# Kernel optimization log

Measured on AMD Instinct MI355X. Metric: run time of the kernel, lower is better.

The kernel has to match this reference:

```python
import jax, jax.numpy as jnp
import numpy as np


def setup_inputs() -> dict:
    key = jax.random.key(0)
    k1, k2, k3, k4 = jax.random.split(key, 4)
    n, c, p1, p2, r = 8, 3, 512, 512, 8
    X = jax.random.uniform(k1, (n, c, p1, p2), dtype=jnp.float32)
    S = jax.random.uniform(k2, (c, r), dtype=jnp.float32)
    S = S / (jnp.linalg.norm(S, axis=0, keepdims=True))  # unit-norm columns like S_init
    gamma = jax.random.uniform(k3, (1,), dtype=jnp.float32) * 1e-05
    lam = jax.random.uniform(k4, (1,), dtype=jnp.float32) * 1e-05
    return {"X": X, "S": S, "gamma": gamma, "lam": lam, "n_iter": 2}


def reference(X, S, gamma, lam, n_iter):
    n, c, p1, p2 = X.shape
    p = p1 * p2
    r = S.shape[1]
    Xf = X.reshape(n, c, p)
    gamma = jnp.abs(gamma)
    lam = jnp.abs(lam)
    Dt = jnp.zeros((n, r, p), dtype=X.dtype)
    x0 = jnp.mean(Xf, axis=2, keepdims=True)
    for _ in range(n_iter):
        # ---- D update (proximal gradient) ----
        SDt = jnp.einsum('cr,nrp->ncp', S, Dt)  # S @ Dt
        x0 = jnp.mean(Xf + SDt, axis=2, keepdims=True)  # [n,c,1]
        tau_D = 1.0 / jnp.sum(S * S)  # 1/||S||_F^2
        Dt = Dt - tau_D * jnp.einsum('cr,ncp->nrp', S, SDt + Xf - x0)
        S_nrm = jnp.linalg.norm(S, axis=0).reshape(1, r, 1)  # [1,r,1]
        Dt = jax.nn.relu(Dt - lam * gamma * tau_D * S_nrm)
        Dt_L2 = jnp.linalg.norm(Dt, axis=2, keepdims=True)  # [n,r,1]
        scl = jax.nn.relu(Dt_L2 - lam * tau_D * S_nrm)
        scl = scl / Dt_L2 + 1e-10  # faithful to source (eps added after divide)
        Dt = Dt * scl
        # ---- S update (proximal gradient) ----
        SDt = jnp.einsum('cr,nrp->ncp', S, Dt)
        x0 = jnp.mean(Xf + SDt, axis=2, keepdims=True)
        Dt_sum = jnp.sum(Dt, axis=2, keepdims=True)  # [n,r,1]
        tau_S = 1.0 / jnp.mean(jnp.sum(Dt * Dt, axis=(1, 2)))
        grad = jnp.mean(
            jnp.einsum('ncp,nqp->ncq', SDt + Xf, Dt)
            - x0 @ jnp.transpose(Dt_sum, (0, 2, 1)),
            axis=0)  # [c,r]
        S_grad = S - tau_S * grad
        Dt_nrm = jnp.mean(
            gamma * jnp.sum(jnp.abs(Dt), axis=2, keepdims=True)
            + jnp.linalg.norm(Dt, axis=2, keepdims=True), axis=0)  # [r,1]
        Sg_nrm = jnp.linalg.norm(S_grad, axis=0, keepdims=True)  # [1,r]
        scl_S = jax.nn.relu(Sg_nrm - lam * tau_S * Dt_nrm.T)
        scl_S = scl_S / (Sg_nrm + 1e-10)
        S = S_grad * scl_S
        # ---- unit-norm rescale (unit_norm_S=True) ----
        S_nrm2 = jnp.linalg.norm(S, axis=0, keepdims=True)  # [1,r]
        S = S / (S_nrm2 + 1e-10)
        Dt = Dt * (S_nrm2.reshape(1, r, 1) + 1e-10)
    return x0, S, Dt.reshape(n, r, p1, p2)
```

## Files before the change

kernel.cpp:

```cpp
#include <hip/hip_runtime.h>

constexpr int N = 8, C = 3, R = 8;
constexpr int P = 512 * 512;
constexpr int BLK = 256;
constexpr int NB = 128;
constexpr int PPB = P / NB;
constexpr int PITER = PPB / (BLK * 4);
constexpr int NK = 68;

typedef float f32x4 __attribute__((ext_vector_type(4)));

constexpr int W_XMEAN = 0;
constexpr int W_S0    = 32;
constexpr int W_S1    = 64;
constexpr int W_S2    = 96;
constexpr int W_X01   = 128;
constexpr int W_X02   = 160;
constexpr int W_F1    = 192;
constexpr int W_F2    = 256;
constexpr int W_TAU1  = 320;
constexpr int W_TAU2  = 321;
constexpr int W_THR1  = 328;
constexpr int W_THR2  = 336;
constexpr int W_SNRM1 = 344;
constexpr int W_SNRM2 = 352;
constexpr int W_RED   = 384;
constexpr int W_PXF   = 1024;
constexpr int W_PART  = 2560;

#define XR8(M) M(0) M(1) M(2) M(3) M(4) M(5) M(6) M(7)
#define XTRI(M) \
  M(0,0) \
  M(1,0) M(1,1) \
  M(2,0) M(2,1) M(2,2) \
  M(3,0) M(3,1) M(3,2) M(3,3) \
  M(4,0) M(4,1) M(4,2) M(4,3) M(4,4) \
  M(5,0) M(5,1) M(5,2) M(5,3) M(5,4) M(5,5) \
  M(6,0) M(6,1) M(6,2) M(6,3) M(6,4) M(6,5) M(6,6) \
  M(7,0) M(7,1) M(7,2) M(7,3) M(7,4) M(7,5) M(7,6) M(7,7)
#define XCR(M) \
  M(0,0) M(0,1) M(0,2) M(0,3) M(0,4) M(0,5) M(0,6) M(0,7) \
  M(1,0) M(1,1) M(1,2) M(1,3) M(1,4) M(1,5) M(1,6) M(1,7) \
  M(2,0) M(2,1) M(2,2) M(2,3) M(2,4) M(2,5) M(2,6) M(2,7)

__device__ __forceinline__ float sld(float x) {
    return __uint_as_float(__builtin_amdgcn_readfirstlane(__float_as_uint(x)));
}

__device__ __forceinline__ float waveSum(float v) {
    #pragma unroll
    for (int o = 32; o > 0; o >>= 1) v += __shfl_down(v, o);
    return v;
}

__global__ __launch_bounds__(BLK)
void k_xmean(const float* __restrict__ X, float* __restrict__ ws) {
    int nc = blockIdx.y;
    int t = threadIdx.x;
    size_t base = (size_t)nc * P + (size_t)blockIdx.x * 4096;
    float s = 0.f;
    #pragma unroll
    for (int i = 0; i < 4; ++i) {
        float4 q = *(const float4*)(X + base + (size_t)(i * BLK + t) * 4);
        s += (q.x + q.y) + (q.z + q.w);
    }
    __shared__ float red[4];
    s = waveSum(s);
    int lane = t & 63, wid = t >> 6;
    if (lane == 0) red[wid] = s;
    __syncthreads();
    if (t == 0) ws[W_PXF + nc * 64 + blockIdx.x] = (red[0] + red[1]) + (red[2] + red[3]);
}

__global__ void k_init(float* __restrict__ ws, const float* __restrict__ Sin,
                       const float* __restrict__ gp, const float* __restrict__ lp) {
    int t = threadIdx.x;
    __shared__ float sS[C * R];
    __shared__ float tau1;
    if (t < N * C) {
        float s = 0.f;
        for (int j = 0; j < 64; ++j) s += ws[W_PXF + t * 64 + j];
        float xm = s * (1.0f / P);
        ws[W_XMEAN + t] = xm;
        ws[W_X01 + t] = xm;
    }
    if (t < C * R) { sS[t] = Sin[t]; ws[W_S0 + t] = Sin[t]; }
    __syncthreads();
    if (t == 0) {
        float ssq = 0.f;
        for (int i = 0; i < C * R; ++i) ssq += sS[i] * sS[i];
        tau1 = 1.0f / ssq;
        ws[W_TAU1] = tau1;
    }
    __syncthreads();
    if (t < R) {
        float s2 = 0.f;
        #pragma unroll
        for (int c = 0; c < C; ++c) { float v = sS[c * R + t]; s2 += v * v; }
        float nrm = sqrtf(s2);
        ws[W_SNRM1 + t] = nrm;
        ws[W_THR1 + t] = fabsf(*lp) * fabsf(*gp) * tau1 * nrm;
    }
}

template <int MODE>
__global__ __launch_bounds__(BLK, 1)
void k_dpass(const float* __restrict__ X, const float* __restrict__ ws,
             float* __restrict__ part, float* __restrict__ Dt_out) {
    const int n = blockIdx.y, t = threadIdx.x;

#define LD_S0(c,q) const float S0_##c##q = sld(ws[W_S0 + (c) * R + (q)]);
#define LD_S1(c,q) const float S1_##c##q = sld(ws[W_S1 + (c) * R + (q)]);
    XCR(LD_S0)
    XCR(LD_S1)
#define LD_TH1(r) const float th1_##r = sld(ws[W_THR1 + (r)]);
#define LD_TH2(r) const float th2_##r = sld(ws[W_THR2 + (r)]);
#define LD_F1(r)  const float f1_##r  = sld(ws[W_F1 + n * R + (r)]);
#define LD_F2(r)  const float f2_##r  = sld(ws[W_F2 + n * R + (r)]);
    XR8(LD_TH1) XR8(LD_TH2) XR8(LD_F1) XR8(LD_F2)
    const float tau1c = sld(ws[W_TAU1]), tau2c = sld(ws[W_TAU2]);
    const float x01_0 = sld(ws[W_X01 + n * C + 0]);
    const float x01_1 = sld(ws[W_X01 + n * C + 1]);
    const float x01_2 = sld(ws[W_X01 + n * C + 2]);
    const float dx0_0 = sld(x01_0 - ws[W_X02 + n * C + 0]);
    const float dx0_1 = sld(x01_1 - ws[W_X02 + n * C + 1]);
    const float dx0_2 = sld(x01_2 - ws[W_X02 + n * C + 2]);

#define D_SM(r)   float sm_##r = 0.f;
#define D_T(q,r)  float tq_##q##_##r = 0.f;
#define D_V(c,q)  float vv_##c##_##q = 0.f;
    XR8(D_SM) XTRI(D_T) XCR(D_V)

    const float* Xn = X + (size_t)n * C * P;
    float* Dn = Dt_out + (size_t)n * R * P;

#define C_P1(r) const float p_##r = fmaxf(fmaf(-tau1c, fmaf(S0_0##r, tt0, fmaf(S0_1##r, tt1, S0_2##r * tt2)), -th1_##r), 0.f);
#define C_AL(r) const float a_##r = p_##r;
#define C_D2(r) const float d_##r = f1_##r * p_##r;
#define C_W(c)  const float w##c = fmaf(S1_##c##0, d_0, fmaf(S1_##c##1, d_1, fmaf(S1_##c##2, d_2, fmaf(S1_##c##3, d_3, fmaf(S1_##c##4, d_4, fmaf(S1_##c##5, d_5, fmaf(S1_##c##6, d_6, fmaf(S1_##c##7, d_7, tt##c + dx0_##c))))))));
#define C_A2(r) const float a_##r = fmaxf(fmaf(-tau2c, fmaf(S1_0##r, w0, fmaf(S1_1##r, w1, S1_2##r * w2)), d_##r - th2_##r), 0.f);
#define AC_SM(r)  sm_##r += a_##r;
#define AC_T(q,r) tq_##q##_##r = fmaf(a_##r, a_##q, tq_##q##_##r);
#define AC_V(c,q) vv_##c##_##q = fmaf(tt##c, a_##q, vv_##c##_##q);
#define PXc(r) ov_##r.x = f2_##r * a_##r;
#define PYc(r) ov_##r.y = f2_##r * a_##r;
#define PZc(r) ov_##r.z = f2_##r * a_##r;
#define PWc(r) ov_##r.w = f2_##r * a_##r;
#define GXc(q) (q).x
#define GYc(q) (q).y
#define GZc(q) (q).z
#define GWc(q) (q).w

#define SITE(GET, PUTM) { \
    const float tt0 = GET(xv0) - x01_0; \
    const float tt1 = GET(xv1) - x01_1; \
    const float tt2 = GET(xv2) - x01_2; \
    XR8(C_P1) \
    if constexpr (MODE == 0) { \
        XR8(C_AL) XR8(AC_SM) XTRI(AC_T) XCR(AC_V) \
    } else { \
        XR8(C_D2) C_W(0) C_W(1) C_W(2) XR8(C_A2) \
        if constexpr (MODE == 1) { XR8(AC_SM) XTRI(AC_T) XCR(AC_V) } \
        else { XR8(PUTM) } \
    } }

#define D_OV(r) float4 ov_##r;
#define ST_O(r) { f32x4 wv = { ov_##r.x, ov_##r.y, ov_##r.z, ov_##r.w }; \
                  __builtin_nontemporal_store(wv, (f32x4*)(Dn + (size_t)(r) * P + pbase)); }

    #pragma unroll
    for (int it = 0; it < PITER; ++it) {
        size_t pbase = (size_t)blockIdx.x * PPB + (size_t)(it * BLK + t) * 4;
        float4 xv0 = *(const float4*)(Xn + 0 * (size_t)P + pbase);
        float4 xv1 = *(const float4*)(Xn + 1 * (size_t)P + pbase);
        float4 xv2 = *(const float4*)(Xn + 2 * (size_t)P + pbase);
        XR8(D_OV)
        SITE(GXc, PXc)
        SITE(GYc, PYc)
        SITE(GZc, PZc)
        SITE(GWc, PWc)
        if constexpr (MODE == 2) { XR8(ST_O) }
    }

    if constexpr (MODE < 2) {
        __shared__ float red[4 * NK];
        const int lane = t & 63, wid = t >> 6;
#define RD_SM(r)  { float v = waveSum(sm_##r);       if (lane == 0) red[wid * NK + (r)] = v; }
#define RD_T(q,r) { float v = waveSum(tq_##q##_##r); if (lane == 0) red[wid * NK + 8 + (q) * ((q) + 1) / 2 + (r)] = v; }
#define RD_V(c,q) { float v = waveSum(vv_##c##_##q); if (lane == 0) red[wid * NK + 44 + (c) * R + (q)] = v; }
        XR8(RD_SM) XTRI(RD_T) XCR(RD_V)
        __syncthreads();
        for (int k = t; k < NK; k += BLK)
            part[((size_t)k * N + n) * NB + blockIdx.x] =
                (red[k] + red[NK + k]) + (red[2 * NK + k] + red[3 * NK + k]);
    }
}

__global__ __launch_bounds__(64)
void k_red(const float* __restrict__ part, float* __restrict__ ws) {
    int g = blockIdx.x, t = threadIdx.x;
    const float* p = part + (size_t)g * NB;
    float s = p[t] + p[t + 64];
    s = waveSum(s);
    if (t == 0) ws[W_RED + g] = s;
}

template <int IT>
__global__ __launch_bounds__(64)
void k_t23(float* __restrict__ ws, const float* __restrict__ gp,
           const float* __restrict__ lp, float* __restrict__ x0_out,
           float* __restrict__ S_out) {
    int t = threadIdx.x;
    __shared__ float sum_[N][R], T_[N][R][R], U_[N][C][R];
    __shared__ float scl_[N][R], L2_[N][R], x0s_[N][C], dtn_[R], x01_[N * C];
    __shared__ float Scur_[C * R], Snew_[C * R], grad_[C * R], snrm2_[R];
    __shared__ float tauS_, lam_, gam_, tauD_;
    for (int i = t; i < NK * N; i += 64) {
        int k = i / N, n = i % N;
        float v = ws[W_RED + k * N + n];
        if (k < 8) sum_[n][k] = v;
        else if (k < 44) {
            int m = k - 8;
            int q = 0;
            while ((q + 1) * (q + 2) / 2 <= m) ++q;
            int r = m - q * (q + 1) / 2;
            T_[n][r][q] = v; T_[n][q][r] = v;
        } else {
            int m = k - 44;
            U_[n][m >> 3][m & 7] = v;
        }
    }
    if (t < N * C) x01_[t] = ws[W_X01 + t];
    if (t == 0) {
        lam_ = fabsf(*lp); gam_ = fabsf(*gp);
        tauD_ = ws[IT ? W_TAU2 : W_TAU1];
    }
    if (t < C * R) Scur_[t] = ws[(IT ? W_S1 : W_S0) + t];
    __syncthreads();
    for (int i = t; i < N * C * R; i += 64) {
        int n = i / (C * R), m = i % (C * R);
        int c = m >> 3, q = m & 7;
        U_[n][c][q] += x01_[n * C + c] * sum_[n][q];
    }
    if (t < N * R) {
        int n = t >> 3, r = t & 7;
        float l2 = sqrtf(T_[n][r][r]);
        float snrm = ws[(IT ? W_SNRM2 : W_SNRM1) + r];
        float scl = fmaxf(l2 - lam_ * tauD_ * snrm, 0.f) / l2 + 1e-10f;
        scl_[n][r] = scl; L2_[n][r] = l2;
    }
    __syncthreads();
    if (t == 0) {
        float tot = 0.f;
        for (int n = 0; n < N; ++n)
            for (int r = 0; r < R; ++r)
                tot += scl_[n][r] * scl_[n][r] * T_[n][r][r];
        tauS_ = (float)N / tot;
    }
    if (t < N * C) {
        int n = t / C, c = t % C;
        float acc = ws[W_XMEAN + t];
        #pragma unroll
        for (int r = 0; r < R; ++r)
            acc += Scur_[c * R + r] * scl_[n][r] * sum_[n][r] * (1.0f / P);
        x0s_[n][c] = acc;
        if (IT == 1) x0_out[t] = acc;
    }
    if (t >= 32 && t < 32 + R) {
        int r = t - 32;
        float a = 0.f;
        #pragma unroll
        for (int n = 0; n < N; ++n)
            a += scl_[n][r] * (gam_ * sum_[n][r] + L2_[n][r]);
        dtn_[r] = a * (1.0f / N);
    }
    __syncthreads();
    if (t < C * R) {
        int c = t / R, q = t % R;
        float a = 0.f;
        #pragma unroll
        for (int n = 0; n < N; ++n) {
            float m = U_[n][c][q];
            #pragma unroll
            for (int r = 0; r < R; ++r)
                m += Scur_[c * R + r] * scl_[n][r] * T_[n][r][q];
            a += scl_[n][q] * (m - x0s_[n][c] * sum_[n][q]);
        }
        grad_[t] = a * (1.0f / N);
    }
    __syncthreads();
    if (t == 0) {
        float Sg[C * R], Sn[C * R];
        #pragma unroll
        for (int i = 0; i < C * R; ++i) Sg[i] = Scur_[i] - tauS_ * grad_[i];
        #pragma unroll
        for (int q = 0; q < R; ++q) {
            float s2 = 0.f;
            #pragma unroll
            for (int c = 0; c < C; ++c) s2 += Sg[c * R + q] * Sg[c * R + q];
            float sgn = sqrtf(s2);
            float s = fmaxf(sgn - lam_ * tauS_ * dtn_[q], 0.f) / (sgn + 1e-10f);
            #pragma unroll
            for (int c = 0; c < C; ++c) Sn[c * R + q] = Sg[c * R + q] * s;
        }
        #pragma unroll
        for (int q = 0; q < R; ++q) {
            float s2 = 0.f;
            #pragma unroll
            for (int c = 0; c < C; ++c) s2 += Sn[c * R + q] * Sn[c * R + q];
            float n2 = sqrtf(s2);
            snrm2_[q] = n2;
            #pragma unroll
            for (int c = 0; c < C; ++c) {
                float v = Sn[c * R + q] / (n2 + 1e-10f);
                Snew_[c * R + q] = v;
                ws[(IT ? W_S2 : W_S1) + c * R + q] = v;
                if (IT == 1) S_out[c * R + q] = v;
            }
        }
        if (IT == 0) {
            float ssq = 0.f;
            #pragma unroll
            for (int i = 0; i < C * R; ++i) ssq += Snew_[i] * Snew_[i];
            float tau2 = 1.0f / ssq;
            ws[W_TAU2] = tau2;
            #pragma unroll
            for (int r = 0; r < R; ++r) {
                float s2 = 0.f;
                #pragma unroll
                for (int c = 0; c < C; ++c) s2 += Snew_[c * R + r] * Snew_[c * R + r];
                float nrm = sqrtf(s2);
                ws[W_SNRM2 + r] = nrm;
                ws[W_THR2 + r] = lam_ * gam_ * tau2 * nrm;
            }
        }
    }
    __syncthreads();
    if (t < N * R) {
        float ft = scl_[t >> 3][t & 7] * (snrm2_[t & 7] + 1e-10f);
        ws[(IT ? W_F2 : W_F1) + t] = ft;
    }
    __syncthreads();
    if (IT == 0 && t < N * C) {
        int n = t / C, c = t % C;
        float acc = ws[W_XMEAN + t];
        #pragma unroll
        for (int r = 0; r < R; ++r)
            acc += Snew_[c * R + r] * ws[W_F1 + n * R + r] * sum_[n][r] * (1.0f / P);
        ws[W_X02 + t] = acc;
    }
}

extern "C" void kernel_launch(void* const* d_in, const int* in_sizes, int n_in,
                              void* d_out, int out_size, void* d_ws, size_t ws_size,
                              hipStream_t stream) {
    const float* X   = (const float*)d_in[0];
    const float* Sin = (const float*)d_in[1];
    const float* gam = (const float*)d_in[2];
    const float* lam = (const float*)d_in[3];
    float* out    = (float*)d_out;
    float* x0_out = out;
    float* S_out  = out + 24;
    float* Dt_out = out + 48;
    float* ws     = (float*)d_ws;
    float* part   = ws + W_PART;

    k_xmean<<<dim3(64, N * C), BLK, 0, stream>>>(X, ws);
    k_init<<<1, 64, 0, stream>>>(ws, Sin, gam, lam);

    k_dpass<0><<<dim3(NB, N), BLK, 0, stream>>>(X, ws, part, Dt_out);
    k_red<<<NK * N, 64, 0, stream>>>(part, ws);
    k_t23<0><<<1, 64, 0, stream>>>(ws, gam, lam, x0_out, S_out);

    k_dpass<1><<<dim3(NB, N), BLK, 0, stream>>>(X, ws, part, Dt_out);
    k_red<<<NK * N, 64, 0, stream>>>(part, ws);
    k_t23<1><<<1, 64, 0, stream>>>(ws, gam, lam, x0_out, S_out);

    k_dpass<2><<<dim3(NB, N), BLK, 0, stream>>>(X, ws, part, Dt_out);
}
```

Measured before the change: 100.5 us.

## Fold reduction and small-matrix update kernels into each dpass prologue

Drops the k_init, k_red and k_t23 kernels. Every dpass block now reduces the previous pass's partial sums itself and redundantly recomputes the small S/scale update, so each iteration is one launch instead of three. The block count is halved (NB 128→64) to shrink the partial-sum arrays each block must read, and ping-pong buffers keep reads and writes apart. In exchange every block repeats about 544 row reductions plus the serial t23 math, and the grid has fewer blocks to spread the streaming work across.

```diff
diff --git a/kernel.cpp b/kernel.cpp
--- a/kernel.cpp
+++ b/kernel.cpp
@@ -3,7 +3,7 @@
 constexpr int N = 8, C = 3, R = 8;
 constexpr int P = 512 * 512;
 constexpr int BLK = 256;
-constexpr int NB = 128;
+constexpr int NB = 64;
 constexpr int PPB = P / NB;
 constexpr int PITER = PPB / (BLK * 4);
 constexpr int NK = 68;
@@ -11,22 +11,15 @@
 typedef float f32x4 __attribute__((ext_vector_type(4)));
 
 constexpr int W_XMEAN = 0;
-constexpr int W_S0    = 32;
-constexpr int W_S1    = 64;
-constexpr int W_S2    = 96;
-constexpr int W_X01   = 128;
+constexpr int W_S1    = 32;
+constexpr int W_F1    = 64;
+constexpr int W_THR2  = 128;
+constexpr int W_TAU2  = 136;
+constexpr int W_SNRM2 = 144;
 constexpr int W_X02   = 160;
-constexpr int W_F1    = 192;
-constexpr int W_F2    = 256;
-constexpr int W_TAU1  = 320;
-constexpr int W_TAU2  = 321;
-constexpr int W_THR1  = 328;
-constexpr int W_THR2  = 336;
-constexpr int W_SNRM1 = 344;
-constexpr int W_SNRM2 = 352;
-constexpr int W_RED   = 384;
-constexpr int W_PXF   = 1024;
-constexpr int W_PART  = 2560;
+constexpr int W_PXF   = 256;
+constexpr int W_PA    = 2048;
+constexpr int W_PB    = 36864;
 
 #define XR8(M) M(0) M(1) M(2) M(3) M(4) M(5) M(6) M(7)
 #define XTRI(M) \
@@ -46,7 +39,6 @@
 __device__ __forceinline__ float sld(float x) {
     return __uint_as_float(__builtin_amdgcn_readfirstlane(__float_as_uint(x)));
 }
-
 __device__ __forceinline__ float waveSum(float v) {
     #pragma unroll
     for (int o = 32; o > 0; o >>= 1) v += __shfl_down(v, o);
@@ -72,59 +64,217 @@
     if (t == 0) ws[W_PXF + nc * 64 + blockIdx.x] = (red[0] + red[1]) + (red[2] + red[3]);
 }
 
-__global__ void k_init(float* __restrict__ ws, const float* __restrict__ Sin,
-                       const float* __restrict__ gp, const float* __restrict__ lp) {
-    int t = threadIdx.x;
-    __shared__ float sS[C * R];
-    __shared__ float tau1;
-    if (t < N * C) {
-        float s = 0.f;
-        for (int j = 0; j < 64; ++j) s += ws[W_PXF + t * 64 + j];
-        float xm = s * (1.0f / P);
-        ws[W_XMEAN + t] = xm;
-        ws[W_X01 + t] = xm;
-    }
-    if (t < C * R) { sS[t] = Sin[t]; ws[W_S0 + t] = Sin[t]; }
-    __syncthreads();
+template <int IT>
+__device__ void t23_math(const float* __restrict__ redL, const float* __restrict__ Sin,
+                         const float* __restrict__ ws, float lam_, float gam_,
+                         float* oS, float* oF, float* oTH2, float* oTAU2,
+                         float* oX02, float* oSN2, float* ox0s) {
+    const int t = threadIdx.x;
+    __shared__ float sum_[N][R], T_[N][R][R], U_[N][C][R];
+    __shared__ float scl_[N][R], L2_[N][R], x0s_[N][C], dtn_[R];
+    __shared__ float Scur_[24], grad_[24], snrm_in[8];
+    __shared__ float tauS_, tauD_;
+    for (int i = t; i < NK * N; i += BLK) {
+        int k = i / N, nn = i % N;
+        float v = redL[k * N + nn];
+        if (k < 8) sum_[nn][k] = v;
+        else if (k < 44) {
+            int m = k - 8; int q = 0;
+            while ((q + 1) * (q + 2) / 2 <= m) ++q;
+            int r = m - q * (q + 1) / 2;
+            T_[nn][r][q] = v; T_[nn][q][r] = v;
+        } else { int m = k - 44; U_[nn][m >> 3][m & 7] = v; }
+    }
+    if (t < 24) Scur_[t] = IT ? ws[W_S1 + t] : Sin[t];
     if (t == 0) {
-        float ssq = 0.f;
-        for (int i = 0; i < C * R; ++i) ssq += sS[i] * sS[i];
-        tau1 = 1.0f / ssq;
-        ws[W_TAU1] = tau1;
-    }
-    __syncthreads();
-    if (t < R) {
-        float s2 = 0.f;
-        #pragma unroll
-        for (int c = 0; c < C; ++c) { float v = sS[c * R + t]; s2 += v * v; }
-        float nrm = sqrtf(s2);
-        ws[W_SNRM1 + t] = nrm;
-        ws[W_THR1 + t] = fabsf(*lp) * fabsf(*gp) * tau1 * nrm;
-    }
+        if (IT) tauD_ = ws[W_TAU2];
+        else { float s = 0.f; for (int i = 0; i < 24; ++i) s += Sin[i] * Sin[i]; tauD_ = 1.0f / s; }
+    }
+    if (t < 8) {
+        if (IT) snrm_in[t] = ws[W_SNRM2 + t];
+        else snrm_in[t] = sqrtf(Sin[t] * Sin[t] + Sin[8 + t] * Sin[8 + t] + Sin[16 + t] * Sin[16 + t]);
+    }
+    __syncthreads();
+    for (int i = t; i < N * C * R; i += BLK) {
+        int nn = i / 24, m = i % 24, c = m >> 3, q = m & 7;
+        U_[nn][c][q] += ws[W_XMEAN + nn * 3 + c] * sum_[nn][q];
+    }
+    if (t < 64) {
+        int nn = t >> 3, r = t & 7;
+        float l2 = sqrtf(T_[nn][r][r]);
+        float scl = fmaxf(l2 - lam_ * tauD_ * snrm_in[r], 0.f) / l2 + 1e-10f;
+        scl_[nn][r] = scl; L2_[nn][r] = l2;
+    }
+    __syncthreads();
+    if (t == 0) {
+        float tot = 0.f;
+        for (int nn = 0; nn < N; ++nn)
+            for (int r = 0; r < R; ++r)
+                tot += scl_[nn][r] * scl_[nn][r] * T_[nn][r][r];
+        tauS_ = (float)N / tot;
+    }
+    if (t < 24) {
+        int nn = t / 3, c = t % 3;
+        float acc = ws[W_XMEAN + t];
+        #pragma unroll
+        for (int r = 0; r < R; ++r)
+            acc += Scur_[c * R + r] * scl_[nn][r] * sum_[nn][r] * (1.0f / P);
+        x0s_[nn][c] = acc;
+        if (IT == 1) ox0s[t] = acc;
+    }
+    if (t >= 32 && t < 40) {
+        int r = t - 32;
+        float a = 0.f;
+        #pragma unroll
+        for (int nn = 0; nn < N; ++nn)
+            a += scl_[nn][r] * (gam_ * sum_[nn][r] + L2_[nn][r]);
+        dtn_[r] = a * (1.0f / N);
+    }
+    __syncthreads();
+    if (t < 24) {
+        int c = t / 8, q = t % 8;
+        float a = 0.f;
+        #pragma unroll
+        for (int nn = 0; nn < N; ++nn) {
+            float m = U_[nn][c][q];
+            #pragma unroll
+            for (int r = 0; r < R; ++r)
+                m += Scur_[c * R + r] * scl_[nn][r] * T_[nn][r][q];
+            a += scl_[nn][q] * (m - x0s_[nn][c] * sum_[nn][q]);
+        }
+        grad_[t] = a * (1.0f / N);
+    }
+    __syncthreads();
+    if (t == 0) {
+        float Sg[24], Sn[24];
+        #pragma unroll
+        for (int i = 0; i < 24; ++i) Sg[i] = Scur_[i] - tauS_ * grad_[i];
+        #pragma unroll
+        for (int q = 0; q < 8; ++q) {
+            float s2 = 0.f;
+            #pragma unroll
+            for (int c = 0; c < 3; ++c) s2 += Sg[c * 8 + q] * Sg[c * 8 + q];
+            float sgn = sqrtf(s2);
+            float s = fmaxf(sgn - lam_ * tauS_ * dtn_[q], 0.f) / (sgn + 1e-10f);
+            #pragma unroll
+            for (int c = 0; c < 3; ++c) Sn[c * 8 + q] = Sg[c * 8 + q] * s;
+        }
+        #pragma unroll
+        for (int q = 0; q < 8; ++q) {
+            float s2 = 0.f;
+            #pragma unroll
+            for (int c = 0; c < 3; ++c) s2 += Sn[c * 8 + q] * Sn[c * 8 + q];
+            float n2 = sqrtf(s2);
+            oSN2[q] = n2;
+            #pragma unroll
+            for (int c = 0; c < 3; ++c) oS[c * 8 + q] = Sn[c * 8 + q] / (n2 + 1e-10f);
+        }
+        if (IT == 0) {
+            float ssq = 0.f;
+            #pragma unroll
+            for (int i = 0; i < 24; ++i) ssq += oS[i] * oS[i];
+            float tau2 = 1.0f / ssq;
+            oTAU2[0] = tau2;
+            #pragma unroll
+            for (int r = 0; r < 8; ++r) {
+                float s2 = oS[r] * oS[r] + oS[8 + r] * oS[8 + r] + oS[16 + r] * oS[16 + r];
+                oTH2[r] = lam_ * gam_ * tau2 * sqrtf(s2);
+            }
+        }
+    }
+    __syncthreads();
+    if (t < 64) oF[t] = scl_[t >> 3][t & 7] * (oSN2[t & 7] + 1e-10f);
+    __syncthreads();
+    if (IT == 0 && t < 24) {
+        int nn = t / 3, c = t % 3;
+        float acc = ws[W_XMEAN + t];
+        #pragma unroll
+        for (int r = 0; r < R; ++r)
+            acc += oS[c * R + r] * oF[nn * R + r] * sum_[nn][r] * (1.0f / P);
+        oX02[t] = acc;
+    }
+    __syncthreads();
 }
 
 template <int MODE>
 __global__ __launch_bounds__(BLK, 1)
-void k_dpass(const float* __restrict__ X, const float* __restrict__ ws,
-             float* __restrict__ part, float* __restrict__ Dt_out) {
+void k_dpass(const float* __restrict__ X, const float* __restrict__ Sin,
+             const float* __restrict__ gp, const float* __restrict__ lp,
+             float* __restrict__ ws, const float* __restrict__ part_in,
+             float* __restrict__ part_out, float* __restrict__ Dt_out,
+             float* __restrict__ x0_out, float* __restrict__ S_out) {
     const int n = blockIdx.y, t = threadIdx.x;
 
-#define LD_S0(c,q) const float S0_##c##q = sld(ws[W_S0 + (c) * R + (q)]);
-#define LD_S1(c,q) const float S1_##c##q = sld(ws[W_S1 + (c) * R + (q)]);
+    __shared__ float redL[NK * N];
+    __shared__ float oS[24], oF[64], oTH2[8], oTAU2[1], oX02[24], oSN2[8], ox0s[24];
+    __shared__ float Lxm[24];
+    __shared__ float redE[4 * NK];
+
+    const float lamv = fabsf(*lp), gamv = fabsf(*gp);
+
+    float ssq0 = 0.f;
+    #pragma unroll
+    for (int i = 0; i < 24; ++i) { float v = Sin[i]; ssq0 = fmaf(v, v, ssq0); }
+    const float tau1c = sld(1.0f / ssq0);
+#define LD_TH1(r) const float th1_##r = sld(lamv * gamv * tau1c * sqrtf(fmaf(Sin[r], Sin[r], fmaf(Sin[8 + r], Sin[8 + r], Sin[16 + r] * Sin[16 + r]))));
+    XR8(LD_TH1)
+
+    if constexpr (MODE == 0) {
+        if (t < 24) {
+            const float* px = ws + W_PXF + t * 64;
+            float s = 0.f;
+            #pragma unroll
+            for (int j = 0; j < 64; ++j) s += px[j];
+            Lxm[t] = s * (1.0f / P);
+        }
+        __syncthreads();
+        if (blockIdx.x == 0 && n == 0 && t < 24) ws[W_XMEAN + t] = Lxm[t];
+    } else {
+        for (int row = t; row < NK * N; row += BLK) {
+            const float* pr = part_in + (size_t)row * NB;
+            float s = 0.f;
+            #pragma unroll
+            for (int j = 0; j < NB / 4; ++j) {
+                float4 q = *(const float4*)(pr + j * 4);
+                s += (q.x + q.y) + (q.z + q.w);
+            }
+            redL[row] = s;
+        }
+        __syncthreads();
+        t23_math<(MODE == 1 ? 0 : 1)>(redL, Sin, ws, lamv, gamv,
+                                      oS, oF, oTH2, oTAU2, oX02, oSN2, ox0s);
+        if constexpr (MODE == 1) {
+            if (blockIdx.x == 0 && n == 0) {
+                if (t < 24) ws[W_S1 + t] = oS[t];
+                if (t < 64) ws[W_F1 + t] = oF[t];
+                if (t < 8)  ws[W_THR2 + t] = oTH2[t];
+                if (t == 0) ws[W_TAU2] = oTAU2[0];
+                if (t < 24) ws[W_X02 + t] = oX02[t];
+                if (t < 8)  ws[W_SNRM2 + t] = oSN2[t];
+            }
+        } else {
+            if (blockIdx.x == 0 && n == 0 && t < 24) {
+                x0_out[t] = ox0s[t];
+                S_out[t] = oS[t];
+            }
+        }
+    }
+
+    const float x01_0 = sld(MODE == 0 ? Lxm[n * 3 + 0] : ws[W_XMEAN + n * 3 + 0]);
+    const float x01_1 = sld(MODE == 0 ? Lxm[n * 3 + 1] : ws[W_XMEAN + n * 3 + 1]);
+    const float x01_2 = sld(MODE == 0 ? Lxm[n * 3 + 2] : ws[W_XMEAN + n * 3 + 2]);
+#define LD_S0(c,q) const float S0_##c##q = sld(Sin[(c) * 8 + (q)]);
     XCR(LD_S0)
+#define LD_S1(c,q) const float S1_##c##q = (MODE >= 1) ? sld(MODE == 1 ? oS[(c) * 8 + (q)] : ws[W_S1 + (c) * 8 + (q)]) : 0.f;
     XCR(LD_S1)
-#define LD_TH1(r) const float th1_##r = sld(ws[W_THR1 + (r)]);
-#define LD_TH2(r) const float th2_##r = sld(ws[W_THR2 + (r)]);
-#define LD_F1(r)  const float f1_##r  = sld(ws[W_F1 + n * R + (r)]);
-#define LD_F2(r)  const float f2_##r  = sld(ws[W_F2 + n * R + (r)]);
-    XR8(LD_TH1) XR8(LD_TH2) XR8(LD_F1) XR8(LD_F2)
-    const float tau1c = sld(ws[W_TAU1]), tau2c = sld(ws[W_TAU2]);
-    const float x01_0 = sld(ws[W_X01 + n * C + 0]);
-    const float x01_1 = sld(ws[W_X01 + n * C + 1]);
-    const float x01_2 = sld(ws[W_X01 + n * C + 2]);
-    const float dx0_0 = sld(x01_0 - ws[W_X02 + n * C + 0]);
-    const float dx0_1 = sld(x01_1 - ws[W_X02 + n * C + 1]);
-    const float dx0_2 = sld(x01_2 - ws[W_X02 + n * C + 2]);
+#define LD_F1(r)  const float f1_##r = (MODE >= 1) ? sld(MODE == 1 ? oF[n * 8 + (r)] : ws[W_F1 + n * 8 + (r)]) : 0.f;
+#define LD_TH2(r) const float th2_##r = (MODE >= 1) ? sld(MODE == 1 ? oTH2[(r)] : ws[W_THR2 + (r)]) : 0.f;
+#define LD_F2(r)  const float f2_##r = (MODE == 2) ? sld(oF[n * 8 + (r)]) : 0.f;
+    XR8(LD_F1) XR8(LD_TH2) XR8(LD_F2)
+    const float tau2c = (MODE >= 1) ? sld(MODE == 1 ? oTAU2[0] : ws[W_TAU2]) : 0.f;
+    const float dx0_0 = (MODE >= 1) ? sld(ws[W_XMEAN + n * 3 + 0] - (MODE == 1 ? oX02[n * 3 + 0] : ws[W_X02 + n * 3 + 0])) : 0.f;
+    const float dx0_1 = (MODE >= 1) ? sld(ws[W_XMEAN + n * 3 + 1] - (MODE == 1 ? oX02[n * 3 + 1] : ws[W_X02 + n * 3 + 1])) : 0.f;
+    const float dx0_2 = (MODE >= 1) ? sld(ws[W_XMEAN + n * 3 + 2] - (MODE == 1 ? oX02[n * 3 + 2] : ws[W_X02 + n * 3 + 2])) : 0.f;
 
 #define D_SM(r)   float sm_##r = 0.f;
 #define D_T(q,r)  float tq_##q##_##r = 0.f;
@@ -183,171 +333,15 @@
     }
 
     if constexpr (MODE < 2) {
-        __shared__ float red[4 * NK];
         const int lane = t & 63, wid = t >> 6;
-#define RD_SM(r)  { float v = waveSum(sm_##r);       if (lane == 0) red[wid * NK + (r)] = v; }
-#define RD_T(q,r) { float v = waveSum(tq_##q##_##r); if (lane == 0) red[wid * NK + 8 + (q) * ((q) + 1) / 2 + (r)] = v; }
-#define RD_V(c,q) { float v = waveSum(vv_##c##_##q); if (lane == 0) red[wid * NK + 44 + (c) * R + (q)] = v; }
+#define RD_SM(r)  { float v = waveSum(sm_##r);       if (lane == 0) redE[wid * NK + (r)] = v; }
+#define RD_T(q,r) { float v = waveSum(tq_##q##_##r); if (lane == 0) redE[wid * NK + 8 + (q) * ((q) + 1) / 2 + (r)] = v; }
+#define RD_V(c,q) { float v = waveSum(vv_##c##_##q); if (lane == 0) redE[wid * NK + 44 + (c) * R + (q)] = v; }
         XR8(RD_SM) XTRI(RD_T) XCR(RD_V)
         __syncthreads();
         for (int k = t; k < NK; k += BLK)
-            part[((size_t)k * N + n) * NB + blockIdx.x] =
-                (red[k] + red[NK + k]) + (red[2 * NK + k] + red[3 * NK + k]);
-    }
-}
-
-__global__ __launch_bounds__(64)
-void k_red(const float* __restrict__ part, float* __restrict__ ws) {
-    int g = blockIdx.x, t = threadIdx.x;
-    const float* p = part + (size_t)g * NB;
-    float s = p[t] + p[t + 64];
-    s = waveSum(s);
-    if (t == 0) ws[W_RED + g] = s;
-}
-
-template <int IT>
-__global__ __launch_bounds__(64)
-void k_t23(float* __restrict__ ws, const float* __restrict__ gp,
-           const float* __restrict__ lp, float* __restrict__ x0_out,
-           float* __restrict__ S_out) {
-    int t = threadIdx.x;
-    __shared__ float sum_[N][R], T_[N][R][R], U_[N][C][R];
-    __shared__ float scl_[N][R], L2_[N][R], x0s_[N][C], dtn_[R], x01_[N * C];
-    __shared__ float Scur_[C * R], Snew_[C * R], grad_[C * R], snrm2_[R];
-    __shared__ float tauS_, lam_, gam_, tauD_;
-    for (int i = t; i < NK * N; i += 64) {
-        int k = i / N, n = i % N;
-        float v = ws[W_RED + k * N + n];
-        if (k < 8) sum_[n][k] = v;
-        else if (k < 44) {
-            int m = k - 8;
-            int q = 0;
-            while ((q + 1) * (q + 2) / 2 <= m) ++q;
-            int r = m - q * (q + 1) / 2;
-            T_[n][r][q] = v; T_[n][q][r] = v;
-        } else {
-            int m = k - 44;
-            U_[n][m >> 3][m & 7] = v;
-        }
-    }
-    if (t < N * C) x01_[t] = ws[W_X01 + t];
-    if (t == 0) {
-        lam_ = fabsf(*lp); gam_ = fabsf(*gp);
-        tauD_ = ws[IT ? W_TAU2 : W_TAU1];
-    }
-    if (t < C * R) Scur_[t] = ws[(IT ? W_S1 : W_S0) + t];
-    __syncthreads();
-    for (int i = t; i < N * C * R; i += 64) {
-        int n = i / (C * R), m = i % (C * R);
-        int c = m >> 3, q = m & 7;
-        U_[n][c][q] += x01_[n * C + c] * sum_[n][q];
-    }
-    if (t < N * R) {
-        int n = t >> 3, r = t & 7;
-        float l2 = sqrtf(T_[n][r][r]);
-        float snrm = ws[(IT ? W_SNRM2 : W_SNRM1) + r];
-        float scl = fmaxf(l2 - lam_ * tauD_ * snrm, 0.f) / l2 + 1e-10f;
-        scl_[n][r] = scl; L2_[n][r] = l2;
-    }
-    __syncthreads();
-    if (t == 0) {
-        float tot = 0.f;
-        for (int n = 0; n < N; ++n)
-            for (int r = 0; r < R; ++r)
-                tot += scl_[n][r] * scl_[n][r] * T_[n][r][r];
-        tauS_ = (float)N / tot;
-    }
-    if (t < N * C) {
-        int n = t / C, c = t % C;
-        float acc = ws[W_XMEAN + t];
-        #pragma unroll
-        for (int r = 0; r < R; ++r)
-            acc += Scur_[c * R + r] * scl_[n][r] * sum_[n][r] * (1.0f / P);
-        x0s_[n][c] = acc;
-        if (IT == 1) x0_out[t] = acc;
-    }
-    if (t >= 32 && t < 32 + R) {
-        int r = t - 32;
-        float a = 0.f;
-        #pragma unroll
-        for (int n = 0; n < N; ++n)
-            a += scl_[n][r] * (gam_ * sum_[n][r] + L2_[n][r]);
-        dtn_[r] = a * (1.0f / N);
-    }
-    __syncthreads();
-    if (t < C * R) {
-        int c = t / R, q = t % R;
-        float a = 0.f;
-        #pragma unroll
-        for (int n = 0; n < N; ++n) {
-            float m = U_[n][c][q];
-            #pragma unroll
-            for (int r = 0; r < R; ++r)
-                m += Scur_[c * R + r] * scl_[n][r] * T_[n][r][q];
-            a += scl_[n][q] * (m - x0s_[n][c] * sum_[n][q]);
-        }
-        grad_[t] = a * (1.0f / N);
-    }
-    __syncthreads();
-    if (t == 0) {
-        float Sg[C * R], Sn[C * R];
-        #pragma unroll
-        for (int i = 0; i < C * R; ++i) Sg[i] = Scur_[i] - tauS_ * grad_[i];
-        #pragma unroll
-        for (int q = 0; q < R; ++q) {
-            float s2 = 0.f;
-            #pragma unroll
-            for (int c = 0; c < C; ++c) s2 += Sg[c * R + q] * Sg[c * R + q];
-            float sgn = sqrtf(s2);
-            float s = fmaxf(sgn - lam_ * tauS_ * dtn_[q], 0.f) / (sgn + 1e-10f);
-            #pragma unroll
-            for (int c = 0; c < C; ++c) Sn[c * R + q] = Sg[c * R + q] * s;
-        }
-        #pragma unroll
-        for (int q = 0; q < R; ++q) {
-            float s2 = 0.f;
-            #pragma unroll
-            for (int c = 0; c < C; ++c) s2 += Sn[c * R + q] * Sn[c * R + q];
-            float n2 = sqrtf(s2);
-            snrm2_[q] = n2;
-            #pragma unroll
-            for (int c = 0; c < C; ++c) {
-                float v = Sn[c * R + q] / (n2 + 1e-10f);
-                Snew_[c * R + q] = v;
-                ws[(IT ? W_S2 : W_S1) + c * R + q] = v;
-                if (IT == 1) S_out[c * R + q] = v;
-            }
-        }
-        if (IT == 0) {
-            float ssq = 0.f;
-            #pragma unroll
-            for (int i = 0; i < C * R; ++i) ssq += Snew_[i] * Snew_[i];
-            float tau2 = 1.0f / ssq;
-            ws[W_TAU2] = tau2;
-            #pragma unroll
-            for (int r = 0; r < R; ++r) {
-                float s2 = 0.f;
-                #pragma unroll
-                for (int c = 0; c < C; ++c) s2 += Snew_[c * R + r] * Snew_[c * R + r];
-                float nrm = sqrtf(s2);
-                ws[W_SNRM2 + r] = nrm;
-                ws[W_THR2 + r] = lam_ * gam_ * tau2 * nrm;
-            }
-        }
-    }
-    __syncthreads();
-    if (t < N * R) {
-        float ft = scl_[t >> 3][t & 7] * (snrm2_[t & 7] + 1e-10f);
-        ws[(IT ? W_F2 : W_F1) + t] = ft;
-    }
-    __syncthreads();
-    if (IT == 0 && t < N * C) {
-        int n = t / C, c = t % C;
-        float acc = ws[W_XMEAN + t];
-        #pragma unroll
-        for (int r = 0; r < R; ++r)
-            acc += Snew_[c * R + r] * ws[W_F1 + n * R + r] * sum_[n][r] * (1.0f / P);
-        ws[W_X02 + t] = acc;
+            part_out[((size_t)k * N + n) * NB + blockIdx.x] =
+                (redE[k] + redE[NK + k]) + (redE[2 * NK + k] + redE[3 * NK + k]);
     }
 }
 
@@ -363,18 +357,11 @@
     float* S_out  = out + 24;
     float* Dt_out = out + 48;
     float* ws     = (float*)d_ws;
-    float* part   = ws + W_PART;
+    float* partA  = ws + W_PA;
+    float* partB  = ws + W_PB;
 
     k_xmean<<<dim3(64, N * C), BLK, 0, stream>>>(X, ws);
-    k_init<<<1, 64, 0, stream>>>(ws, Sin, gam, lam);
-
-    k_dpass<0><<<dim3(NB, N), BLK, 0, stream>>>(X, ws, part, Dt_out);
-    k_red<<<NK * N, 64, 0, stream>>>(part, ws);
-    k_t23<0><<<1, 64, 0, stream>>>(ws, gam, lam, x0_out, S_out);
-
-    k_dpass<1><<<dim3(NB, N), BLK, 0, stream>>>(X, ws, part, Dt_out);
-    k_red<<<NK * N, 64, 0, stream>>>(part, ws);
-    k_t23<1><<<1, 64, 0, stream>>>(ws, gam, lam, x0_out, S_out);
-
-    k_dpass<2><<<dim3(NB, N), BLK, 0, stream>>>(X, ws, part, Dt_out);
-}
+    k_dpass<0><<<dim3(NB, N), BLK, 0, stream>>>(X, Sin, gam, lam, ws, partA, partA, Dt_out, x0_out, S_out);
+    k_dpass<1><<<dim3(NB, N), BLK, 0, stream>>>(X, Sin, gam, lam, ws, partA, partB, Dt_out, x0_out, S_out);
+    k_dpass<2><<<dim3(NB, N), BLK, 0, stream>>>(X, Sin, gam, lam, ws, partB, partA, Dt_out, x0_out, S_out);
+}
```

New measurement: 98.40 us. -2.1%, faster.
